# Optimization experiments

Hardware: AMD Instinct MI355X
Metric: run time of the kernel (lower is better)

## Reference

```python
import jax, jax.numpy as jnp
import numpy as np

NZ, NX, NB = 512, 512, 512
LAYERS = [6, 40, 40, 40, 40, 1]
WIDTH = [6, 40, 80, 160, 320, 1]
PI = np.float32(np.pi)


def _block_diag_mask(n_blocks, r, c):
    m = np.zeros((n_blocks * r, n_blocks * c), np.float32)
    for i in range(n_blocks):
        m[i * r:(i + 1) * r, i * c:(i + 1) * c] = 1.0
    return jnp.asarray(m)

# masks for layers l=2 (2 blocks of 40x80) and l=3 (4 blocks of 40x80)
_M0 = _block_diag_mask(2, 40, 80)   # (80, 160)
_M1 = _block_diag_mask(4, 40, 80)   # (160, 320)


def _xavier(key, shape):
    lim = np.sqrt(6.0 / (shape[0] + shape[1])).astype(np.float32)
    return jax.random.uniform(key, shape, jnp.float32, -lim, lim)


def setup_inputs():
    key = jax.random.key(0)
    ks = jax.random.split(key, 20)
    d = {}
    d["xi_coord"] = jax.random.uniform(ks[0], (NX, 3), jnp.float32)
    d["xi_wts"] = jax.random.uniform(ks[1], (NX,), jnp.float32) / NX
    d["xb_coord"] = jax.random.uniform(ks[2], (NB, 3), jnp.float32)
    d["xb_wts"] = jax.random.uniform(ks[3], (NB,), jnp.float32) / NB
    nrm = jax.random.normal(ks[4], (NB, 3), jnp.float32)
    d["xb_normal"] = nrm / jnp.linalg.norm(nrm, axis=1, keepdims=True)
    d["z_coord"] = jax.random.uniform(ks[5], (NZ, 3), jnp.float32)
    for i, (fi, fo) in enumerate(zip(WIDTH[:-1], WIDTH[1:])):
        d[f"W{i}"] = _xavier(ks[6 + i], (fi, fo))
        d[f"b{i}"] = 0.1 * jax.random.normal(ks[11 + i], (1, fo), jnp.float32)
    d["xb_btype"] = jax.random.randint(ks[16], (NB,), 0, 3)
    d["case_index"] = 0
    return d


def _bsnn(X, Ws, bs):
    # layers 0,1 dense; layers 2,3 block-diag masked; final linear
    X = jnp.sin(X @ Ws[0] + bs[0])
    X = jnp.sin(X @ Ws[1] + bs[1])
    X = jnp.sin(X @ (Ws[2] * _M0) + bs[2])
    X = jnp.sin(X @ (Ws[3] * _M1) + bs[3])
    return X @ Ws[4] + bs[4]


def _f_src(x, case_index):   # problem.f : (N,3) -> (N,)
    c = np.float32(case_index + 1)
    return jnp.sin(PI * c * x[:, 0]) * jnp.sin(PI * x[:, 1]) * jnp.sin(PI * x[:, 2])


def _g_bc(x, btype, case_index):  # problem.g : (N,3),(N,) -> (N,)
    c = np.float32(case_index + 1)
    return jnp.sin(c * jnp.sum(x, axis=1)) * (1.0 + 0.1 * btype.astype(x.dtype))


def _a_coef(x):   # problem.a : (N,3) -> (N,)
    return 1.0 + 0.5 * jnp.cos(x[:, 0])


def _tile(x, z):
    # torch: X = x.repeat(nz,1); Y = cat([z[i].repeat(nx,1)]) -> row = z_idx*nx + x_idx
    nx, nz = x.shape[0], z.shape[0]
    return jnp.concatenate([jnp.tile(x, (nz, 1)), jnp.repeat(z, nx, axis=0)], axis=1)


def reference(xi_coord, xi_wts, xb_coord, xb_wts, xb_normal, z_coord,
              W0, b0, W1, b1, W2, b2, W3, b3, W4, b4, xb_btype, case_index):
    Ws = [W0, W1, W2, W3, W4]
    bs = [b0, b1, b2, b3, b4]
    nz, nx, nb = z_coord.shape[0], xi_coord.shape[0], xb_coord.shape[0]

    # ---- interior quadrature: fG_quad[z] = sum_x f(x) G(x,z) w(x) ----
    inp_i = _tile(xi_coord, z_coord)                      # (nz*nx, 6)
    G_i = _bsnn(inp_i, Ws, bs).reshape(nz, nx)            # (nz, nx)
    f_i = _f_src(xi_coord, case_index)                    # (nx,)
    fG_quad = (G_i * f_i[None, :]) @ xi_wts               # (nz,)

    # ---- boundary quadrature: gGn_quad[z] = sum_b a g (grad_x G . n) w(b) ----
    inp_b = _tile(xb_coord, z_coord)                      # (nz*nb, 6)
    net = lambda X: _bsnn(X, Ws, bs)
    Gb, vjp = jax.vjp(net, inp_b)
    dG = vjp(jnp.ones_like(Gb))[0][:, :3].reshape(nz, nb, 3)  # grad wrt x-part
    Gn = jnp.einsum('znc,nc->zn', dG, xb_normal)          # (nz, nb)
    g_b = _g_bc(xb_coord, xb_btype, case_index)           # (nb,)
    a_b = _a_coef(xb_coord)                               # (nb,)
    gGn_quad = (Gn * (a_b * g_b)[None, :]) @ xb_wts       # (nz,)

    return (fG_quad - gGn_quad)[:, None]                  # (nz, 1)
```

## Files before the change

kernel.cpp:

```cpp
#include <hip/hip_runtime.h>

#define PI_F 3.14159265358979f

typedef _Float16 f16;
typedef _Float16 f16x8 __attribute__((ext_vector_type(8)));
typedef float f32x4 __attribute__((ext_vector_type(4)));

#define MFMA16(A,B,C) __builtin_amdgcn_mfma_f32_16x16x32_f16(A,B,C,0,0,0)


__global__ __launch_bounds__(256)
void pack_kernel(const float* __restrict__ W0, const float* __restrict__ b0,
                 const float* __restrict__ W1, const float* __restrict__ b1,
                 const float* __restrict__ W2, const float* __restrict__ b2,
                 const float* __restrict__ W3, const float* __restrict__ b3,
                 const float* __restrict__ xb_coord, const float* __restrict__ xb_wts,
                 const int* __restrict__ xb_btype,
                 const float* __restrict__ xi_coord, const float* __restrict__ xi_wts,
                 const int* __restrict__ case_index,
                 f16* __restrict__ wp, float* __restrict__ fp)
{
  const int idx = blockIdx.x*256 + threadIdx.x;
  if (idx < 1536) {
    const int n = idx >> 5, k = idx & 31;
    float v = 0.f;
    if (n < 40) {
      if (k < 6) v = W0[k*40+n];
      else if (k < 12) { const float w = W0[(k-6)*40+n]; v = w - (float)(f16)w; }
      else if (k < 18) v = W0[(k-12)*40+n];
      else if (k == 18) v = b0[n];
      else if (k == 19) { const float w = b0[n]; v = w - (float)(f16)w; }
    }
    wp[idx] = (f16)v;
  } else if (idx < 6656) {
    const int r = idx - 1536, n = r >> 6, k = r & 63;
    float v = 0.f;
    if (k < 40) v = W1[k*80+n];
    else if (k == 40) v = b1[n];
    else if (k == 41) { const float w = b1[n]; v = w - (float)(f16)w; }
    wp[idx] = (f16)v;
  } else if (idx < 18944) {
    const int r = idx - 6656, g = r / 3072, q = r - g*3072, n = q >> 6, k = q & 63;
    float v = 0.f;
    if (n < 40) {
      if (k < 40) v = W2[(40*(g>>1)+k)*160 + 40*g + n];
      else if (k == 40) v = b2[40*g+n];
      else if (k == 41) { const float w = b2[40*g+n]; v = w - (float)(f16)w; }
    }
    wp[idx] = (f16)v;
  } else if (idx < 39424) {
    const int r = idx - 18944, g = r / 5120, q = r - g*5120, n = q >> 6, k = q & 63;
    float v = 0.f;
    if (k < 40) v = W3[(40*g+k)*320 + 80*g + n];
    else if (k == 40) v = b3[80*g+n];
    else if (k == 41) { const float w = b3[80*g+n]; v = w - (float)(f16)w; }
    wp[idx] = (f16)v;
  } else if (idx < 39936) {
    const int p = idx - 39424;
    const float c = (float)(case_index[0]+1);
    const float x0=xb_coord[p*3], x1=xb_coord[p*3+1], x2=xb_coord[p*3+2];
    fp[p] = __sinf(c*(x0+x1+x2)) * (1.f + 0.1f*(float)xb_btype[p])
          * (1.f + 0.5f*__cosf(x0)) * xb_wts[p];
  } else if (idx < 40448) {
    const int p = idx - 39936;
    const float c = (float)(case_index[0]+1);
    fp[512+p] = __sinf(PI_F*c*xi_coord[p*3]) * __sinf(PI_F*xi_coord[p*3+1])
              * __sinf(PI_F*xi_coord[p*3+2]) * xi_wts[p];
  }
}

template<bool BND>
__global__ __launch_bounds__(256)
void net_mfma(const float* __restrict__ coord,
              const float* __restrict__ nrm,
              const float* __restrict__ z_coord,
              const float* __restrict__ W4, const float* __restrict__ b4,
              const f16* __restrict__ wp, const float* __restrict__ fp,
              float* __restrict__ out)
{
  __shared__ f16 sm[4*6528];
  const int tid = threadIdx.x, lane = tid & 63;
  const int wv = __builtin_amdgcn_readfirstlane(tid >> 6);
  f16* XW = sm + wv*6528;
  f16* X0 = XW;
  f16* X1 = XW + 1152;
  f16* X2 = XW + 3072;
  const int r16 = lane & 15, quad = lane >> 4;

  const int bid = blockIdx.x;
  const int z = bid >> 1;
  const int HP = BND ? 8 : 4;
  const int pbeg = (bid & 1) * HP, pend = pbeg + HP;

  const float zc0 = z_coord[z*3+0], zc1 = z_coord[z*3+1], zc2 = z_coord[z*3+2];
  const f16* W0P = wp;
  const f16* W1P = wp + 1536;
  const f16* W2P = wp + 6656;
  const f16* W3P = wp + 18944;
  const float* FAC = BND ? fp : (fp + 512);
  const float b4v = b4[0];
  const f32x4 czero = {0.f,0.f,0.f,0.f};

  {
    f16x8 zz = {(f16)0.f,(f16)0.f,(f16)0.f,(f16)0.f,(f16)0.f,(f16)0.f,(f16)0.f,(f16)0.f};
    for (int i = lane; i < 816; i += 64) ((f16x8*)XW)[i] = zz;
    if (quad == 0) {
      const f16 fv = (f16)((BND && (r16 & 1)) ? 0.f : 1.f);
      X0[r16*72 + 40] = fv;  X0[r16*72 + 41] = fv;
      X1[r16*120 + 40] = fv; X1[r16*120 + 41] = fv;
      X1[r16*120 + 88] = fv; X1[r16*120 + 89] = fv;
      #pragma unroll
      for (int g = 0; g < 4; g++) {
        X2[r16*216 + 48*g + 40] = fv; X2[r16*216 + 48*g + 41] = fv;
      }
    }
  }

  float wacc = 0.f;

  for (int panel = pbeg; panel < pend; panel++) {
    const int rowbase = panel*64 + wv*16;

    {
      float i0,i1,i2,i3,i4,i5,fv;
      if (BND) {
        const int r = rowbase + r16;
        const int p = r >> 1;
        if (r & 1) { i0=nrm[p*3]; i1=nrm[p*3+1]; i2=nrm[p*3+2]; i3=0.f;i4=0.f;i5=0.f; fv=0.f; }
        else       { i0=coord[p*3]; i1=coord[p*3+1]; i2=coord[p*3+2]; i3=zc0;i4=zc1;i5=zc2; fv=1.f; }
      } else {
        const int p = rowbase + r16;
        i0=coord[p*3]; i1=coord[p*3+1]; i2=coord[p*3+2]; i3=zc0;i4=zc1;i5=zc2; fv=1.f;
      }
      const f16 H0=(f16)i0,H1=(f16)i1,H2=(f16)i2,H3=(f16)i3,H4=(f16)i4,H5=(f16)i5;
      const f16 L0_=(f16)(i0-(float)H0), L1_=(f16)(i1-(float)H1), L2_=(f16)(i2-(float)H2);
      const f16 L3_=(f16)(i3-(float)H3), L4_=(f16)(i4-(float)H4), L5_=(f16)(i5-(float)H5);
      const f16 FV=(f16)fv, Z=(f16)0.f;
      f16x8 a = {Z,Z,Z,Z,Z,Z,Z,Z};
      if (quad == 0)      { a[0]=H0;a[1]=H1;a[2]=H2;a[3]=H3;a[4]=H4;a[5]=H5;a[6]=H0;a[7]=H1; }
      else if (quad == 1) { a[0]=H2;a[1]=H3;a[2]=H4;a[3]=H5;a[4]=L0_;a[5]=L1_;a[6]=L2_;a[7]=L3_; }
      else if (quad == 2) { a[0]=L4_;a[1]=L5_;a[2]=FV;a[3]=FV; }

      #pragma unroll
      for (int t = 0; t < 3; t++) {
        const f16x8 b = *(const f16x8*)(W0P + (t*16 + r16)*32 + quad*8);
        const f32x4 c = MFMA16(a, b, czero);
        const int col = t*16 + r16;
        if (t < 2 || r16 < 8) {
          if (BND) {
            X0[(quad*4+0)*72 + col] = (f16)__sinf(c[0]);
            X0[(quad*4+1)*72 + col] = (f16)(__cosf(c[0]) * c[1]);
            X0[(quad*4+2)*72 + col] = (f16)__sinf(c[2]);
            X0[(quad*4+3)*72 + col] = (f16)(__cosf(c[2]) * c[3]);
          } else {
            X0[(quad*4+0)*72 + col] = (f16)__sinf(c[0]);
            X0[(quad*4+1)*72 + col] = (f16)__sinf(c[1]);
            X0[(quad*4+2)*72 + col] = (f16)__sinf(c[2]);
            X0[(quad*4+3)*72 + col] = (f16)__sinf(c[3]);
          }
        }
      }
    }

    {
      const f16x8 A0 = *(const f16x8*)(X0 + r16*72 + quad*8);
      const f16x8 A1 = *(const f16x8*)(X0 + r16*72 + 32 + quad*8);
      #pragma unroll
      for (int t = 0; t < 5; t++) {
        const f16* bp = W1P + (t*16 + r16)*64 + quad*8;
        const f16x8 b0 = *(const f16x8*)bp;
        const f16x8 b1 = *(const f16x8*)(bp + 32);
        f32x4 c = MFMA16(A0, b0, czero);
        c = MFMA16(A1, b1, c);
        const int n = t*16 + r16;
        const int col = n + (n >= 40 ? 8 : 0);
        if (BND) {
          X1[(quad*4+0)*120 + col] = (f16)__sinf(c[0]);
          X1[(quad*4+1)*120 + col] = (f16)(__cosf(c[0]) * c[1]);
          X1[(quad*4+2)*120 + col] = (f16)__sinf(c[2]);
          X1[(quad*4+3)*120 + col] = (f16)(__cosf(c[2]) * c[3]);
        } else {
          X1[(quad*4+0)*120 + col] = (f16)__sinf(c[0]);
          X1[(quad*4+1)*120 + col] = (f16)__sinf(c[1]);
          X1[(quad*4+2)*120 + col] = (f16)__sinf(c[2]);
          X1[(quad*4+3)*120 + col] = (f16)__sinf(c[3]);
        }
      }
    }

    #pragma unroll
    for (int g = 0; g < 4; g++) {
      const int h = g >> 1;
      const f16x8 A0 = *(const f16x8*)(X1 + r16*120 + 48*h + quad*8);
      const f16x8 A1 = *(const f16x8*)(X1 + r16*120 + 48*h + 32 + quad*8);
      #pragma unroll
      for (int t = 0; t < 3; t++) {
        const f16* bp = W2P + g*3072 + (t*16 + r16)*64 + quad*8;
        const f16x8 b0 = *(const f16x8*)bp;
        const f16x8 b1 = *(const f16x8*)(bp + 32);
        f32x4 c = MFMA16(A0, b0, czero);
        c = MFMA16(A1, b1, c);
        if (t < 2 || r16 < 8) {
          const int col = 48*g + t*16 + r16;
          if (BND) {
            X2[(quad*4+0)*216 + col] = (f16)__sinf(c[0]);
            X2[(quad*4+1)*216 + col] = (f16)(__cosf(c[0]) * c[1]);
            X2[(quad*4+2)*216 + col] = (f16)__sinf(c[2]);
            X2[(quad*4+3)*216 + col] = (f16)(__cosf(c[2]) * c[3]);
          } else {
            X2[(quad*4+0)*216 + col] = (f16)__sinf(c[0]);
            X2[(quad*4+1)*216 + col] = (f16)__sinf(c[1]);
            X2[(quad*4+2)*216 + col] = (f16)__sinf(c[2]);
            X2[(quad*4+3)*216 + col] = (f16)__sinf(c[3]);
          }
        }
      }
    }

    float p0=0.f, p1=0.f, p2=0.f, p3=0.f;
    #pragma unroll
    for (int g = 0; g < 4; g++) {
      const f16x8 A0 = *(const f16x8*)(X2 + r16*216 + 48*g + quad*8);
      const f16x8 A1 = *(const f16x8*)(X2 + r16*216 + 48*g + 32 + quad*8);
      #pragma unroll
      for (int t = 0; t < 5; t++) {
        const f16* bp = W3P + g*5120 + (t*16 + r16)*64 + quad*8;
        const f16x8 b0 = *(const f16x8*)bp;
        const f16x8 b1 = *(const f16x8*)(bp + 32);
        f32x4 c = MFMA16(A0, b0, czero);
        c = MFMA16(A1, b1, c);
        const float w4 = W4[80*g + t*16 + r16];
        if (BND) {
          p1 += __cosf(c[0]) * c[1] * w4;
          p3 += __cosf(c[2]) * c[3] * w4;
        } else {
          p0 += __sinf(c[0]) * w4;
          p1 += __sinf(c[1]) * w4;
          p2 += __sinf(c[2]) * w4;
          p3 += __sinf(c[3]) * w4;
        }
      }
    }

    #pragma unroll
    for (int m = 1; m < 16; m <<= 1) {
      p1 += __shfl_xor(p1, m);
      p3 += __shfl_xor(p3, m);
      if (!BND) { p0 += __shfl_xor(p0, m); p2 += __shfl_xor(p2, m); }
    }
    if (r16 == 0) {
      if (BND) {
        const int pr = (rowbase >> 1) + quad*2;
        wacc += p1 * FAC[pr] + p3 * FAC[pr+1];
      } else {
        const int r0 = rowbase + quad*4;
        wacc += (p0+b4v)*FAC[r0] + (p1+b4v)*FAC[r0+1]
              + (p2+b4v)*FAC[r0+2] + (p3+b4v)*FAC[r0+3];
      }
    }
  }

  #pragma unroll
  for (int m = 16; m < 64; m <<= 1) wacc += __shfl_xor(wacc, m);
  if (lane == 0) atomicAdd(out + z, BND ? -wacc : wacc);
}

extern "C" void kernel_launch(void* const* d_in, const int* in_sizes, int n_in,
                              void* d_out, int out_size, void* d_ws, size_t ws_size,
                              hipStream_t stream) {
  const float* xi_coord  = (const float*)d_in[0];
  const float* xi_wts    = (const float*)d_in[1];
  const float* xb_coord  = (const float*)d_in[2];
  const float* xb_wts    = (const float*)d_in[3];
  const float* xb_normal = (const float*)d_in[4];
  const float* z_coord   = (const float*)d_in[5];
  const float* W0 = (const float*)d_in[6];
  const float* b0 = (const float*)d_in[7];
  const float* W1 = (const float*)d_in[8];
  const float* b1 = (const float*)d_in[9];
  const float* W2 = (const float*)d_in[10];
  const float* b2 = (const float*)d_in[11];
  const float* W3 = (const float*)d_in[12];
  const float* b3 = (const float*)d_in[13];
  const float* W4 = (const float*)d_in[14];
  const float* b4 = (const float*)d_in[15];
  const int* xb_btype   = (const int*)d_in[16];
  const int* case_index = (const int*)d_in[17];
  float* out = (float*)d_out;
  f16* wp = (f16*)d_ws;
  float* fpf = (float*)((char*)d_ws + 78848);

  hipMemsetAsync(d_out, 0, (size_t)out_size * sizeof(float), stream);

  hipLaunchKernelGGL(pack_kernel, dim3(158), dim3(256), 0, stream,
      W0, b0, W1, b1, W2, b2, W3, b3,
      xb_coord, xb_wts, xb_btype, xi_coord, xi_wts, case_index, wp, fpf);

  hipLaunchKernelGGL((net_mfma<true>), dim3(1024), dim3(256), 0, stream,
      xb_coord, xb_normal, z_coord, W4, b4, wp, fpf, out);
  hipLaunchKernelGGL((net_mfma<false>), dim3(1024), dim3(256), 0, stream,
      xi_coord, xb_normal, z_coord, W4, b4, wp, fpf, out);
}
```

Before: 332.6 us.

## Merge boundary and interior network kernels into one balanced launch

Replaces the two templated launches (boundary and interior) with a single kernel of 3072 blocks that picks its mode from the block index. Boundary work is split into 4-panel chunks so every block does the same amount of work. It also uses sincos for the paired sin/cos evaluations, limits unrolling, and sets launch bounds to 3 blocks per CU to lower register pressure and raise occupancy. The cost is a runtime branch on mode instead of compile-time specialization, and possibly worse scheduling from the reduced unrolling.

```diff
diff --git a/kernel.cpp b/kernel.cpp
--- a/kernel.cpp
+++ b/kernel.cpp
@@ -69,11 +69,9 @@
   }
 }
 
-template<bool BND>
-__global__ __launch_bounds__(256)
-void net_mfma(const float* __restrict__ coord,
-              const float* __restrict__ nrm,
-              const float* __restrict__ z_coord,
+__global__ __launch_bounds__(256, 3)
+void net_mfma(const float* __restrict__ xb_coord, const float* __restrict__ xb_normal,
+              const float* __restrict__ xi_coord, const float* __restrict__ z_coord,
               const float* __restrict__ W4, const float* __restrict__ b4,
               const f16* __restrict__ wp, const float* __restrict__ fp,
               float* __restrict__ out)
@@ -88,16 +86,19 @@
   const int r16 = lane & 15, quad = lane >> 4;
 
   const int bid = blockIdx.x;
-  const int z = bid >> 1;
-  const int HP = BND ? 8 : 4;
-  const int pbeg = (bid & 1) * HP, pend = pbeg + HP;
+  const bool bnd = (bid < 2048);
+  int z, pbeg;
+  const float* coord;
+  if (bnd) { z = bid >> 2; pbeg = (bid & 3) * 4; coord = xb_coord; }
+  else { const int b = bid - 2048; z = b >> 1; pbeg = (b & 1) * 4; coord = xi_coord; }
+  const int pend = pbeg + 4;
 
   const float zc0 = z_coord[z*3+0], zc1 = z_coord[z*3+1], zc2 = z_coord[z*3+2];
   const f16* W0P = wp;
   const f16* W1P = wp + 1536;
   const f16* W2P = wp + 6656;
   const f16* W3P = wp + 18944;
-  const float* FAC = BND ? fp : (fp + 512);
+  const float* FAC = bnd ? fp : (fp + 512);
   const float b4v = b4[0];
   const f32x4 czero = {0.f,0.f,0.f,0.f};
 
@@ -105,7 +106,7 @@
     f16x8 zz = {(f16)0.f,(f16)0.f,(f16)0.f,(f16)0.f,(f16)0.f,(f16)0.f,(f16)0.f,(f16)0.f};
     for (int i = lane; i < 816; i += 64) ((f16x8*)XW)[i] = zz;
     if (quad == 0) {
-      const f16 fv = (f16)((BND && (r16 & 1)) ? 0.f : 1.f);
+      const f16 fv = (f16)((bnd && (r16 & 1)) ? 0.f : 1.f);
       X0[r16*72 + 40] = fv;  X0[r16*72 + 41] = fv;
       X1[r16*120 + 40] = fv; X1[r16*120 + 41] = fv;
       X1[r16*120 + 88] = fv; X1[r16*120 + 89] = fv;
@@ -123,11 +124,13 @@
 
     {
       float i0,i1,i2,i3,i4,i5,fv;
-      if (BND) {
+      if (bnd) {
         const int r = rowbase + r16;
         const int p = r >> 1;
-        if (r & 1) { i0=nrm[p*3]; i1=nrm[p*3+1]; i2=nrm[p*3+2]; i3=0.f;i4=0.f;i5=0.f; fv=0.f; }
-        else       { i0=coord[p*3]; i1=coord[p*3+1]; i2=coord[p*3+2]; i3=zc0;i4=zc1;i5=zc2; fv=1.f; }
+        if (r & 1) { i0=xb_normal[p*3]; i1=xb_normal[p*3+1]; i2=xb_normal[p*3+2];
+                     i3=0.f;i4=0.f;i5=0.f; fv=0.f; }
+        else       { i0=coord[p*3]; i1=coord[p*3+1]; i2=coord[p*3+2];
+                     i3=zc0;i4=zc1;i5=zc2; fv=1.f; }
       } else {
         const int p = rowbase + r16;
         i0=coord[p*3]; i1=coord[p*3+1]; i2=coord[p*3+2]; i3=zc0;i4=zc1;i5=zc2; fv=1.f;
@@ -147,11 +150,14 @@
         const f32x4 c = MFMA16(a, b, czero);
         const int col = t*16 + r16;
         if (t < 2 || r16 < 8) {
-          if (BND) {
-            X0[(quad*4+0)*72 + col] = (f16)__sinf(c[0]);
-            X0[(quad*4+1)*72 + col] = (f16)(__cosf(c[0]) * c[1]);
-            X0[(quad*4+2)*72 + col] = (f16)__sinf(c[2]);
-            X0[(quad*4+3)*72 + col] = (f16)(__cosf(c[2]) * c[3]);
+          if (bnd) {
+            float s0, c0v, s2, c2v;
+            __sincosf(c[0], &s0, &c0v);
+            __sincosf(c[2], &s2, &c2v);
+            X0[(quad*4+0)*72 + col] = (f16)s0;
+            X0[(quad*4+1)*72 + col] = (f16)(c0v * c[1]);
+            X0[(quad*4+2)*72 + col] = (f16)s2;
+            X0[(quad*4+3)*72 + col] = (f16)(c2v * c[3]);
           } else {
             X0[(quad*4+0)*72 + col] = (f16)__sinf(c[0]);
             X0[(quad*4+1)*72 + col] = (f16)__sinf(c[1]);
@@ -165,7 +171,7 @@
     {
       const f16x8 A0 = *(const f16x8*)(X0 + r16*72 + quad*8);
       const f16x8 A1 = *(const f16x8*)(X0 + r16*72 + 32 + quad*8);
-      #pragma unroll
+      #pragma unroll 2
       for (int t = 0; t < 5; t++) {
         const f16* bp = W1P + (t*16 + r16)*64 + quad*8;
         const f16x8 b0 = *(const f16x8*)bp;
@@ -174,11 +180,14 @@
         c = MFMA16(A1, b1, c);
         const int n = t*16 + r16;
         const int col = n + (n >= 40 ? 8 : 0);
-        if (BND) {
-          X1[(quad*4+0)*120 + col] = (f16)__sinf(c[0]);
-          X1[(quad*4+1)*120 + col] = (f16)(__cosf(c[0]) * c[1]);
-          X1[(quad*4+2)*120 + col] = (f16)__sinf(c[2]);
-          X1[(quad*4+3)*120 + col] = (f16)(__cosf(c[2]) * c[3]);
+        if (bnd) {
+          float s0, c0v, s2, c2v;
+          __sincosf(c[0], &s0, &c0v);
+          __sincosf(c[2], &s2, &c2v);
+          X1[(quad*4+0)*120 + col] = (f16)s0;
+          X1[(quad*4+1)*120 + col] = (f16)(c0v * c[1]);
+          X1[(quad*4+2)*120 + col] = (f16)s2;
+          X1[(quad*4+3)*120 + col] = (f16)(c2v * c[3]);
         } else {
           X1[(quad*4+0)*120 + col] = (f16)__sinf(c[0]);
           X1[(quad*4+1)*120 + col] = (f16)__sinf(c[1]);
@@ -188,12 +197,12 @@
       }
     }
 
-    #pragma unroll
+    #pragma unroll 1
     for (int g = 0; g < 4; g++) {
       const int h = g >> 1;
       const f16x8 A0 = *(const f16x8*)(X1 + r16*120 + 48*h + quad*8);
       const f16x8 A1 = *(const f16x8*)(X1 + r16*120 + 48*h + 32 + quad*8);
-      #pragma unroll
+      #pragma unroll 2
       for (int t = 0; t < 3; t++) {
         const f16* bp = W2P + g*3072 + (t*16 + r16)*64 + quad*8;
         const f16x8 b0 = *(const f16x8*)bp;
@@ -202,11 +211,14 @@
         c = MFMA16(A1, b1, c);
         if (t < 2 || r16 < 8) {
           const int col = 48*g + t*16 + r16;
-          if (BND) {
-            X2[(quad*4+0)*216 + col] = (f16)__sinf(c[0]);
-            X2[(quad*4+1)*216 + col] = (f16)(__cosf(c[0]) * c[1]);
-            X2[(quad*4+2)*216 + col] = (f16)__sinf(c[2]);
-            X2[(quad*4+3)*216 + col] = (f16)(__cosf(c[2]) * c[3]);
+          if (bnd) {
+            float s0, c0v, s2, c2v;
+            __sincosf(c[0], &s0, &c0v);
+            __sincosf(c[2], &s2, &c2v);
+            X2[(quad*4+0)*216 + col] = (f16)s0;
+            X2[(quad*4+1)*216 + col] = (f16)(c0v * c[1]);
+            X2[(quad*4+2)*216 + col] = (f16)s2;
+            X2[(quad*4+3)*216 + col] = (f16)(c2v * c[3]);
           } else {
             X2[(quad*4+0)*216 + col] = (f16)__sinf(c[0]);
             X2[(quad*4+1)*216 + col] = (f16)__sinf(c[1]);
@@ -218,11 +230,11 @@
     }
 
     float p0=0.f, p1=0.f, p2=0.f, p3=0.f;
-    #pragma unroll
+    #pragma unroll 1
     for (int g = 0; g < 4; g++) {
       const f16x8 A0 = *(const f16x8*)(X2 + r16*216 + 48*g + quad*8);
       const f16x8 A1 = *(const f16x8*)(X2 + r16*216 + 48*g + 32 + quad*8);
-      #pragma unroll
+      #pragma unroll 2
       for (int t = 0; t < 5; t++) {
         const f16* bp = W3P + g*5120 + (t*16 + r16)*64 + quad*8;
         const f16x8 b0 = *(const f16x8*)bp;
@@ -230,7 +242,7 @@
         f32x4 c = MFMA16(A0, b0, czero);
         c = MFMA16(A1, b1, c);
         const float w4 = W4[80*g + t*16 + r16];
-        if (BND) {
+        if (bnd) {
           p1 += __cosf(c[0]) * c[1] * w4;
           p3 += __cosf(c[2]) * c[3] * w4;
         } else {
@@ -246,10 +258,10 @@
     for (int m = 1; m < 16; m <<= 1) {
       p1 += __shfl_xor(p1, m);
       p3 += __shfl_xor(p3, m);
-      if (!BND) { p0 += __shfl_xor(p0, m); p2 += __shfl_xor(p2, m); }
+      if (!bnd) { p0 += __shfl_xor(p0, m); p2 += __shfl_xor(p2, m); }
     }
     if (r16 == 0) {
-      if (BND) {
+      if (bnd) {
         const int pr = (rowbase >> 1) + quad*2;
         wacc += p1 * FAC[pr] + p3 * FAC[pr+1];
       } else {
@@ -262,7 +274,7 @@
 
   #pragma unroll
   for (int m = 16; m < 64; m <<= 1) wacc += __shfl_xor(wacc, m);
-  if (lane == 0) atomicAdd(out + z, BND ? -wacc : wacc);
+  if (lane == 0) atomicAdd(out + z, bnd ? -wacc : wacc);
 }
 
 extern "C" void kernel_launch(void* const* d_in, const int* in_sizes, int n_in,
@@ -296,8 +308,6 @@
       W0, b0, W1, b1, W2, b2, W3, b3,
       xb_coord, xb_wts, xb_btype, xi_coord, xi_wts, case_index, wp, fpf);
 
-  hipLaunchKernelGGL((net_mfma<true>), dim3(1024), dim3(256), 0, stream,
-      xb_coord, xb_normal, z_coord, W4, b4, wp, fpf, out);
-  hipLaunchKernelGGL((net_mfma<false>), dim3(1024), dim3(256), 0, stream,
-      xi_coord, xb_normal, z_coord, W4, b4, wp, fpf, out);
+  hipLaunchKernelGGL(net_mfma, dim3(3072), dim3(256), 0, stream,
+      xb_coord, xb_normal, xi_coord, z_coord, W4, b4, wp, fpf, out);
 }
```

New measurement: 469.3 us. +41.1%, slower.
